# Kernel tuning notes

Hardware: AMD Instinct MI355X
Metric: run time of the kernel (lower is better)

Reference implementation:

```python
import jax, jax.numpy as jnp
import numpy as np

B, T, D = 2, 2048, 1024
H, DH = 16, 64
WINDOW = 256
SCALE = DH ** -0.5


def setup_inputs() -> dict:
    key = jax.random.key(0)
    ks = jax.random.split(key, 5)
    x = jax.random.normal(ks[0], (B, T, D), dtype=jnp.float32)
    # Linear params (y = x @ W + b form)
    w_qkv = jax.random.normal(ks[1], (D, 3 * D), dtype=jnp.float32) * (D ** -0.5)
    b_qkv = jnp.zeros((3 * D,), dtype=jnp.float32)
    w_out = jax.random.normal(ks[2], (D, D), dtype=jnp.float32) * (D ** -0.5)
    b_out = jnp.zeros((D,), dtype=jnp.float32)
    return {"x": x, "w_qkv": w_qkv, "b_qkv": b_qkv, "w_out": w_out, "b_out": b_out}


def reference(x, w_qkv, b_qkv, w_out, b_out):
    Bs, Ts, Ds = x.shape
    qkv = x @ w_qkv + b_qkv  # [B,T,3D]
    q, k, v = jnp.split(qkv, 3, axis=-1)
    # [B,H,T,dh]
    def heads(t):
        return t.reshape(Bs, Ts, H, DH).transpose(0, 2, 1, 3)
    q, k, v = heads(q), heads(k), heads(v)
    scores = jnp.einsum('bhqd,bhkd->bhqk', q, k) * SCALE
    i = jnp.arange(Ts)[:, None]
    j = jnp.arange(Ts)[None, :]
    # allowed: i - WINDOW <= j <= i  (causal + local window)
    allowed = (j <= i) & (j >= i - WINDOW)
    scores = jnp.where(allowed, scores, -jnp.inf)
    attn = jax.nn.softmax(scores, axis=-1)  # dropout is identity in eval
    out = jnp.einsum('bhqk,bhkd->bhqd', attn, v)
    out = out.transpose(0, 2, 1, 3).reshape(Bs, Ts, Ds)
    return out @ w_out + b_out
```

## Files before the change

### kernel.cpp

```cpp
#include <hip/hip_runtime.h>

#define BN 2
#define T_DIM 2048
#define D_DIM 1024
#define H_N 16
#define DH_N 64
#define WIN 256
#define NROWS (BN * T_DIM)
#define KDIM 1024

typedef __attribute__((ext_vector_type(8))) short bf16x8;
typedef __attribute__((ext_vector_type(4))) float f32x4;
typedef __attribute__((ext_vector_type(8))) unsigned short ushort8;
typedef __attribute__((ext_vector_type(4))) unsigned short u16x4;

static __device__ __forceinline__ unsigned short f2bf(float f) {
  unsigned int u = __float_as_uint(f);
  unsigned int r = (u + 0x7FFFu + ((u >> 16) & 1u)) >> 16;
  return (unsigned short)r;
}

static __device__ __forceinline__ void gl_lds16(const void* g, void* l) {
  __builtin_amdgcn_global_load_lds(
      (const __attribute__((address_space(1))) unsigned int*)g,
      (__attribute__((address_space(3))) unsigned int*)l, 16, 0, 0);
}

#define MFMA16(a, b, c) __builtin_amdgcn_mfma_f32_16x16x32_bf16(a, b, c, 0, 0, 0)

static __device__ __forceinline__ void transpose_tile(
    const float* __restrict__ src, unsigned short* __restrict__ dst, int R,
    int C, int bx, int by, float* tile ) {
  const int t = threadIdx.x;
  const int bc = bx * 64, br = by * 64;
#pragma unroll
  for (int i = 0; i < 16; ++i) {
    int idx = i * 256 + t;
    int r = idx >> 6, c = idx & 63;
    tile[r * 65 + c] = src[(size_t)(br + r) * C + bc + c];
  }
  __syncthreads();
#pragma unroll
  for (int i = 0; i < 16; ++i) {
    int idx = i * 256 + t;
    int r = idx >> 6, c = idx & 63;
    dst[(size_t)(bc + r) * R + br + c] = f2bf(tile[c * 65 + r]);
  }
}

__global__ __launch_bounds__(256) void convert_all(
    const float* __restrict__ x, const float* __restrict__ w_qkv,
    const float* __restrict__ w_out, unsigned short* __restrict__ xbf,
    unsigned short* __restrict__ wqkvt, unsigned short* __restrict__ woutt) {
  __shared__ float tile[64 * 65];
  const int id = blockIdx.x;
  if (id < 2048) {
    int i = (id * 256 + threadIdx.x) * 8;
    float4 a = *(const float4*)(x + i);
    float4 b = *(const float4*)(x + i + 4);
    ushort8 o;
    o[0] = f2bf(a.x); o[1] = f2bf(a.y); o[2] = f2bf(a.z); o[3] = f2bf(a.w);
    o[4] = f2bf(b.x); o[5] = f2bf(b.y); o[6] = f2bf(b.z); o[7] = f2bf(b.w);
    *(ushort8*)(xbf + i) = o;
  } else if (id < 2816) {
    int j = id - 2048;
    transpose_tile(w_qkv, wqkvt, D_DIM, 3 * D_DIM, j % 48, j / 48, tile);
  } else {
    int j = id - 2816;
    transpose_tile(w_out, woutt, D_DIM, D_DIM, j % 16, j / 16, tile);
  }
}

__global__ __launch_bounds__(512) void gemm_qkv_8p(
    const unsigned short* __restrict__ A, const unsigned short* __restrict__ Bt,
    const float* __restrict__ bias, unsigned short* __restrict__ qo,
    unsigned short* __restrict__ ko, unsigned short* __restrict__ vto) {
  __shared__ unsigned short As[2][256 * 64];
  __shared__ unsigned short Bs[2][192 * 64];

  const int tid = threadIdx.x;
  const int w = tid >> 6, l = tid & 63;
  const int wr = w >> 2, wc = w & 3;
  const int l15 = l & 15, kslc = l >> 4;

  const int id = blockIdx.x;
  const int wg = (id & 7) * 32 + (id >> 3);
  const int bx = wg & 15, by = wg >> 4;
  const int r0 = by * 256, c0 = bx * 192;

  const unsigned short* Ag = A + (size_t)r0 * KDIM;
  const unsigned short* Bg = Bt + (size_t)c0 * KDIM;

  f32x4 acc[8][3];
#pragma unroll
  for (int i = 0; i < 8; ++i)
#pragma unroll
    for (int j = 0; j < 3; ++j) acc[i][j] = (f32x4){0.f, 0.f, 0.f, 0.f};

  const int grow = tid >> 3;
  const int gcol = (tid & 7) ^ (grow & 7);

#define STAGE_A(T, BUF, CH)                                                    \
  gl_lds16(Ag + (size_t)((CH)*64 + grow) * KDIM + (T)*64 + gcol * 8,           \
           (char*)&As[BUF][0] + (CH)*8192 + w * 1024)
#define STAGE_B(T, BUF, CH)                                                    \
  gl_lds16(Bg + (size_t)((CH)*64 + grow) * KDIM + (T)*64 + gcol * 8,           \
           (char*)&Bs[BUF][0] + (CH)*8192 + w * 1024)

#define LDA(CB, mi, ks)                                                        \
  (*(const bf16x8*)((const char*)&As[CB][0] +                                  \
                    (wr * 128 + (mi)*16 + l15) * 128 +                         \
                    ((((ks)*4 + kslc) ^ (l15 & 7)) << 4)))
#define LDB(CB, ni, ks)                                                        \
  (*(const bf16x8*)((const char*)&Bs[CB][0] +                                  \
                    (wc * 48 + (ni)*16 + l15) * 128 +                          \
                    ((((ks)*4 + kslc) ^ (l15 & 7)) << 4)))

#define CLUSTER12(B_, A0, A1, A2, A3, B0, B1, B2)                              \
  do {                                                                         \
    __builtin_amdgcn_s_setprio(1);                                             \
    acc[B_ + 0][0] = MFMA16(A0, B0, acc[B_ + 0][0]);                           \
    acc[B_ + 0][1] = MFMA16(A0, B1, acc[B_ + 0][1]);                           \
    acc[B_ + 0][2] = MFMA16(A0, B2, acc[B_ + 0][2]);                           \
    acc[B_ + 1][0] = MFMA16(A1, B0, acc[B_ + 1][0]);                           \
    acc[B_ + 1][1] = MFMA16(A1, B1, acc[B_ + 1][1]);                           \
    acc[B_ + 1][2] = MFMA16(A1, B2, acc[B_ + 1][2]);                           \
    acc[B_ + 2][0] = MFMA16(A2, B0, acc[B_ + 2][0]);                           \
    acc[B_ + 2][1] = MFMA16(A2, B1, acc[B_ + 2][1]);                           \
    acc[B_ + 2][2] = MFMA16(A2, B2, acc[B_ + 2][2]);                           \
    acc[B_ + 3][0] = MFMA16(A3, B0, acc[B_ + 3][0]);                           \
    acc[B_ + 3][1] = MFMA16(A3, B1, acc[B_ + 3][1]);                           \
    acc[B_ + 3][2] = MFMA16(A3, B2, acc[B_ + 3][2]);                           \
    __builtin_amdgcn_s_setprio(0);                                             \
  } while (0)

  STAGE_A(0, 0, 0); STAGE_A(0, 0, 1); STAGE_A(0, 0, 2); STAGE_A(0, 0, 3);
  STAGE_B(0, 0, 0); STAGE_B(0, 0, 1); STAGE_B(0, 0, 2);

#pragma unroll 1
  for (int t = 0; t < 15; ++t) {
    const int cb = t & 1, nb = cb ^ 1;
    STAGE_A(t + 1, nb, 0); STAGE_A(t + 1, nb, 1);
    asm volatile("s_waitcnt vmcnt(2)" ::: "memory");
    __builtin_amdgcn_s_barrier();
    {
      bf16x8 a0 = LDA(cb, 0, 0), a1 = LDA(cb, 1, 0), a2 = LDA(cb, 2, 0),
             a3 = LDA(cb, 3, 0);
      bf16x8 b0 = LDB(cb, 0, 0), b1 = LDB(cb, 1, 0), b2 = LDB(cb, 2, 0);
      CLUSTER12(0, a0, a1, a2, a3, b0, b1, b2);
      __builtin_amdgcn_s_barrier();
      bf16x8 a4 = LDA(cb, 4, 0), a5 = LDA(cb, 5, 0), a6 = LDA(cb, 6, 0),
             a7 = LDA(cb, 7, 0);
      STAGE_A(t + 1, nb, 2); STAGE_A(t + 1, nb, 3);
      __builtin_amdgcn_s_barrier();
      CLUSTER12(4, a4, a5, a6, a7, b0, b1, b2);
      __builtin_amdgcn_s_barrier();
      bf16x8 c0_ = LDA(cb, 0, 1), c1_ = LDA(cb, 1, 1), c2_ = LDA(cb, 2, 1),
             c3_ = LDA(cb, 3, 1);
      bf16x8 d0 = LDB(cb, 0, 1), d1 = LDB(cb, 1, 1), d2 = LDB(cb, 2, 1);
      STAGE_B(t + 1, nb, 0); STAGE_B(t + 1, nb, 1);
      __builtin_amdgcn_s_barrier();
      CLUSTER12(0, c0_, c1_, c2_, c3_, d0, d1, d2);
      __builtin_amdgcn_s_barrier();
      bf16x8 c4 = LDA(cb, 4, 1), c5 = LDA(cb, 5, 1), c6 = LDA(cb, 6, 1),
             c7 = LDA(cb, 7, 1);
      STAGE_B(t + 1, nb, 2);
      __builtin_amdgcn_s_barrier();
      CLUSTER12(4, c4, c5, c6, c7, d0, d1, d2);
      __builtin_amdgcn_s_barrier();
    }
  }
  asm volatile("s_waitcnt vmcnt(0)" ::: "memory");
  __builtin_amdgcn_s_barrier();
  {
    bf16x8 a0 = LDA(1, 0, 0), a1 = LDA(1, 1, 0), a2 = LDA(1, 2, 0),
           a3 = LDA(1, 3, 0);
    bf16x8 b0 = LDB(1, 0, 0), b1 = LDB(1, 1, 0), b2 = LDB(1, 2, 0);
    CLUSTER12(0, a0, a1, a2, a3, b0, b1, b2);
    bf16x8 a4 = LDA(1, 4, 0), a5 = LDA(1, 5, 0), a6 = LDA(1, 6, 0),
           a7 = LDA(1, 7, 0);
    CLUSTER12(4, a4, a5, a6, a7, b0, b1, b2);
    bf16x8 c0_ = LDA(1, 0, 1), c1_ = LDA(1, 1, 1), c2_ = LDA(1, 2, 1),
           c3_ = LDA(1, 3, 1);
    bf16x8 d0 = LDB(1, 0, 1), d1 = LDB(1, 1, 1), d2 = LDB(1, 2, 1);
    CLUSTER12(0, c0_, c1_, c2_, c3_, d0, d1, d2);
    bf16x8 c4 = LDA(1, 4, 1), c5 = LDA(1, 5, 1), c6 = LDA(1, 6, 1),
           c7 = LDA(1, 7, 1);
    CLUSTER12(4, c4, c5, c6, c7, d0, d1, d2);
  }
#undef STAGE_A
#undef STAGE_B
#undef LDA
#undef LDB
#undef CLUSTER12

#pragma unroll
  for (int ni = 0; ni < 3; ++ni) {
    const int col0 = c0 + wc * 48 + ni * 16;
    const int which = col0 >> 10;
    const int h = (col0 >> 6) & 15;
    const int dh = (col0 & 63) + l15;
    const float bv = bias[col0 + l15];
#pragma unroll
    for (int mi = 0; mi < 8; ++mi) {
      int row = r0 + wr * 128 + mi * 16 + (l >> 4) * 4;
      int b_ = row >> 11, t0 = row & 2047;
      if (which == 2) {
        u16x4 pk;
#pragma unroll
        for (int j = 0; j < 4; ++j) pk[j] = f2bf(acc[mi][ni][j] + bv);
        *(u16x4*)(vto + ((size_t)(b_ * H_N + h) * DH_N + dh) * T_DIM + t0) = pk;
      } else {
        float mul = (which == 0) ? 0.125f : 1.0f;
        unsigned short* dst = (which == 0) ? qo : ko;
#pragma unroll
        for (int j = 0; j < 4; ++j)
          dst[((size_t)(b_ * H_N + h) * T_DIM + t0 + j) * DH_N + dh] =
              f2bf((acc[mi][ni][j] + bv) * mul);
      }
    }
  }
}

__global__ __launch_bounds__(256) void gemm_out_p4(
    const unsigned short* __restrict__ A, const unsigned short* __restrict__ Bt,
    const float* __restrict__ bias, float* __restrict__ fo) {
  __shared__ unsigned short As[4][4096];
  __shared__ unsigned short Bs[4][4096];

  const int tid = threadIdx.x;
  const int w = tid >> 6, l = tid & 63;
  const int wr = w >> 1, wc = w & 1;
  const int l15 = l & 15, kslc = l >> 4;

  const int id = blockIdx.x;
  const int wg = (id & 7) * 32 + (id >> 3);
  const int bx = wg & 7, by = wg >> 3;
  const int r0 = by * 128, c0 = bx * 128;

  const unsigned short* Ag = A + (size_t)r0 * KDIM;
  const unsigned short* Bg = Bt + (size_t)c0 * KDIM;

  f32x4 acc[4][4];
#pragma unroll
  for (int i = 0; i < 4; ++i)
#pragma unroll
    for (int j = 0; j < 4; ++j) acc[i][j] = (f32x4){0.f, 0.f, 0.f, 0.f};

  const int srow = l >> 2;
  const int srcslot = (l & 3) ^ ((l >> 3) & 3);

#define STAGE_O(T, BUF)                                                        \
  do {                                                                         \
    const size_t kk0 = (size_t)(T) * 32;                                       \
    gl_lds16(Ag + (size_t)(w * 16 + srow) * KDIM + kk0 + srcslot * 8,          \
             (char*)&As[BUF][0] + w * 1024);                                   \
    gl_lds16(Ag + (size_t)(64 + w * 16 + srow) * KDIM + kk0 + srcslot * 8,     \
             (char*)&As[BUF][0] + (4 + w) * 1024);                             \
    gl_lds16(Bg + (size_t)(w * 16 + srow) * KDIM + kk0 + srcslot * 8,          \
             (char*)&Bs[BUF][0] + w * 1024);                                   \
    gl_lds16(Bg + (size_t)(64 + w * 16 + srow) * KDIM + kk0 + srcslot * 8,     \
             (char*)&Bs[BUF][0] + (4 + w) * 1024);                             \
  } while (0)

#define OCOMPUTE(CB)                                                           \
  do {                                                                         \
    bf16x8 af[4], bfr[4];                                                      \
    _Pragma("unroll") for (int mi = 0; mi < 4; ++mi) {                         \
      int row = wr * 64 + mi * 16 + l15;                                       \
      af[mi] = *(const bf16x8*)((const char*)&As[CB][0] + row * 64 +           \
                                ((kslc ^ ((row >> 1) & 3)) << 4));             \
    }                                                                          \
    _Pragma("unroll") for (int ni = 0; ni < 4; ++ni) {                         \
      int row = wc * 64 + ni * 16 + l15;                                       \
      bfr[ni] = *(const bf16x8*)((const char*)&Bs[CB][0] + row * 64 +          \
                                 ((kslc ^ ((row >> 1) & 3)) << 4));            \
    }                                                                          \
    __builtin_amdgcn_s_setprio(1);                                             \
    _Pragma("unroll") for (int mi = 0; mi < 4; ++mi)                           \
        _Pragma("unroll") for (int ni = 0; ni < 4; ++ni) acc[mi][ni] =         \
            MFMA16(af[mi], bfr[ni], acc[mi][ni]);                              \
    __builtin_amdgcn_s_setprio(0);                                             \
  } while (0)

  STAGE_O(0, 0);
  STAGE_O(1, 1);

  for (int t = 0; t < 30; ++t) {
    STAGE_O(t + 2, (t + 2) & 3);
    asm volatile("s_waitcnt vmcnt(8)" ::: "memory");
    __builtin_amdgcn_s_barrier();
    OCOMPUTE(t & 3);
  }
  asm volatile("s_waitcnt vmcnt(4)" ::: "memory");
  __builtin_amdgcn_s_barrier();
  OCOMPUTE(2);
  asm volatile("s_waitcnt vmcnt(0)" ::: "memory");
  __builtin_amdgcn_s_barrier();
  OCOMPUTE(3);
#undef STAGE_O
#undef OCOMPUTE

#pragma unroll
  for (int mi = 0; mi < 4; ++mi) {
#pragma unroll
    for (int ni = 0; ni < 4; ++ni) {
      int row = r0 + wr * 64 + mi * 16 + (l >> 4) * 4;
      int col = c0 + wc * 64 + ni * 16 + l15;
      float bv = bias[col];
#pragma unroll
      for (int j = 0; j < 4; ++j)
        fo[(size_t)(row + j) * D_DIM + col] = acc[mi][ni][j] + bv;
    }
  }
}

__global__ __launch_bounds__(256) void attn_mono(
    const unsigned short* __restrict__ qbf,
    const unsigned short* __restrict__ kbf,
    const unsigned short* __restrict__ vtbf,
    unsigned short* __restrict__ ctx) {
  __shared__ unsigned short Ks[5 * 4096];
  __shared__ unsigned short Vs[5 * 4096];
  const int tid = threadIdx.x;
  const int w = tid >> 6, l = tid & 63;
  const int g = l >> 4, ln = l & 15;
  const int qt = blockIdx.x & 31;
  const int bh = blockIdx.x >> 5;
  const int q0 = qt * 64;
  const int q_abs = q0 + w * 16 + ln;

  const unsigned short* kp = kbf + (size_t)bh * T_DIM * DH_N;
  const unsigned short* vtp = vtbf + (size_t)bh * DH_N * T_DIM;

  bf16x8 qf0, qf1;
  {
    const unsigned short* qp = qbf + ((size_t)bh * T_DIM + q_abs) * DH_N;
    qf0 = *(const bf16x8*)(qp + g * 8);
    qf1 = *(const bf16x8*)(qp + 32 + g * 8);
  }

#define KAP(row) \
  (32 * (((row) >> 4) & 1) + 8 * (((row)&15) >> 2) + 4 * ((row) >> 5) + ((row)&3))

  const int kt_lo = (q0 >= WIN) ? (q0 - WIN) : 0;
  const int nt = ((q0 - kt_lo) >> 6) + 1;

  for (int i = 0; i < nt; ++i) {
    const int kt = kt_lo + i * 64;
#pragma unroll
    for (int i_ = 0; i_ < 2; ++i_) {
      int chunk = i_ * 256 + tid;
      int row = chunk >> 3, c16 = chunk & 7;
      int sc16 = c16 ^ (row & 7);
      int kap = KAP(row);
      gl_lds16(kp + (size_t)(kt + kap) * DH_N + sc16 * 8,
               (char*)Ks + i * 8192 + chunk * 16);
      gl_lds16(vtp + (size_t)row * T_DIM + kt + sc16 * 8,
               (char*)Vs + i * 8192 + chunk * 16);
    }
  }
  asm volatile("s_waitcnt vmcnt(0)" ::: "memory");
  __builtin_amdgcn_s_barrier();

  f32x4 acc_o[4];
#pragma unroll
  for (int nd = 0; nd < 4; ++nd) acc_o[nd] = (f32x4){0.f, 0.f, 0.f, 0.f};
  float m = -1e30f, lsum = 0.f;

  for (int i = 0; i < nt; ++i) {
    const int kt = kt_lo + i * 64;
    const char* Kb = (const char*)Ks + i * 8192;
    const char* Vb = (const char*)Vs + i * 8192;

    f32x4 sacc[4];
#pragma unroll
    for (int nk = 0; nk < 4; ++nk) sacc[nk] = (f32x4){0.f, 0.f, 0.f, 0.f};
#pragma unroll
    for (int ks = 0; ks < 2; ++ks) {
      bf16x8 qf = ks ? qf1 : qf0;
#pragma unroll
      for (int nk = 0; nk < 4; ++nk) {
        int rrow = nk * 16 + ln;
        int c16 = ks * 4 + g;
        bf16x8 kf =
            *(const bf16x8*)(Kb + rrow * 128 + ((c16 ^ (rrow & 7)) * 16));
        sacc[nk] = MFMA16(kf, qf, sacc[nk]);
      }
    }

    float p[4][4];
    float tm = -1e30f;
#pragma unroll
    for (int nk = 0; nk < 4; ++nk)
#pragma unroll
      for (int j = 0; j < 4; ++j) {
        int k_abs = kt + 32 * (nk & 1) + 8 * g + 4 * (nk >> 1) + j;
        float s = sacc[nk][j];
        bool ok = (k_abs <= q_abs) && (k_abs + WIN >= q_abs);
        s = ok ? s : -1e30f;
        p[nk][j] = s;
        tm = fmaxf(tm, s);
      }
    tm = fmaxf(tm, __shfl_xor(tm, 16, 64));
    tm = fmaxf(tm, __shfl_xor(tm, 32, 64));
    float mn = fmaxf(m, tm);
    float sc = __expf(m - mn);
    float ps = 0.f;
#pragma unroll
    for (int nk = 0; nk < 4; ++nk)
#pragma unroll
      for (int j = 0; j < 4; ++j) {
        p[nk][j] = __expf(p[nk][j] - mn);
        ps += p[nk][j];
      }
    ps += __shfl_xor(ps, 16, 64);
    ps += __shfl_xor(ps, 32, 64);
    lsum = lsum * sc + ps;
    m = mn;
#pragma unroll
    for (int nd = 0; nd < 4; ++nd) {
      acc_o[nd][0] *= sc; acc_o[nd][1] *= sc;
      acc_o[nd][2] *= sc; acc_o[nd][3] *= sc;
    }

    unsigned int pk[4][2];
#pragma unroll
    for (int nk = 0; nk < 4; ++nk) {
      pk[nk][0] = (unsigned)f2bf(p[nk][0]) | ((unsigned)f2bf(p[nk][1]) << 16);
      pk[nk][1] = (unsigned)f2bf(p[nk][2]) | ((unsigned)f2bf(p[nk][3]) << 16);
    }

#pragma unroll
    for (int ks = 0; ks < 2; ++ks) {
      union { unsigned int d[4]; bf16x8 v; } pf;
      pf.d[0] = pk[ks][0];     pf.d[1] = pk[ks][1];
      pf.d[2] = pk[2 + ks][0]; pf.d[3] = pk[2 + ks][1];
#pragma unroll
      for (int nd = 0; nd < 4; ++nd) {
        int drow = nd * 16 + ln;
        int c16 = ks * 4 + g;
        bf16x8 vf =
            *(const bf16x8*)(Vb + drow * 128 + ((c16 ^ (drow & 7)) * 16));
        acc_o[nd] = MFMA16(vf, pf.v, acc_o[nd]);
      }
    }
  }
#undef KAP

  float inv = 1.f / lsum;
  const int b_ = bh >> 4, h = bh & 15;
  unsigned short* op = ctx + ((size_t)b_ * T_DIM + q_abs) * D_DIM + h * DH_N;
#pragma unroll
  for (int nd = 0; nd < 4; ++nd) {
    u16x4 o;
#pragma unroll
    for (int j = 0; j < 4; ++j) o[j] = f2bf(acc_o[nd][j] * inv);
    *(u16x4*)(op + nd * 16 + g * 4) = o;
  }
}

extern "C" void kernel_launch(void* const* d_in, const int* in_sizes, int n_in,
                              void* d_out, int out_size, void* d_ws,
                              size_t ws_size, hipStream_t stream) {
  const float* x = (const float*)d_in[0];
  const float* w_qkv = (const float*)d_in[1];
  const float* b_qkv = (const float*)d_in[2];
  const float* w_out = (const float*)d_in[3];
  const float* b_out = (const float*)d_in[4];
  float* out = (float*)d_out;

  const size_t per = (size_t)BN * H_N * T_DIM * DH_N;
  unsigned short* qbf = (unsigned short*)d_ws;
  unsigned short* kbf = qbf + per;
  unsigned short* vtbf = kbf + per;
  unsigned short* xbf = vtbf + per;
  unsigned short* wqkvt = xbf + (size_t)NROWS * D_DIM;
  unsigned short* woutt = wqkvt + (size_t)3 * D_DIM * D_DIM;
  unsigned short* ctxbf = woutt + (size_t)D_DIM * D_DIM;

  convert_all<<<dim3(3072), dim3(256), 0, stream>>>(x, w_qkv, w_out, xbf,
                                                    wqkvt, woutt);

  gemm_qkv_8p<<<dim3(256), dim3(512), 0, stream>>>(xbf, wqkvt, b_qkv, qbf, kbf,
                                                   vtbf);

  attn_mono<<<dim3(BN * H_N * (T_DIM / 64)), dim3(256), 0, stream>>>(
      qbf, kbf, vtbf, ctxbf);

  gemm_out_p4<<<dim3(256), dim3(256), 0, stream>>>(ctxbf, woutt, b_out, out);
}
```

Measured before the change: 92.28 us.

## Load attention K/V fragments directly from global memory instead of LDS staging

The attention kernel no longer stages the whole K/V window into shared memory with a barrier. Each lane now reads its MFMA K and V^T fragments straight from global memory through precomputed per-lane base pointers. Block indices are also remapped so blocks with the same query tile but different heads run near each other, which should improve L2 locality. This frees LDS and removes the upfront load-and-wait, but every wave now issues its own global loads with no cross-wave reuse and no explicit prefetch, so it depends on cache hits.

Measured after the change: 109.4 us. 18.5% more time.

```diff
diff --git a/kernel.cpp b/kernel.cpp
--- a/kernel.cpp
+++ b/kernel.cpp
@@ -315,18 +315,19 @@
   }
 }
 
-__global__ __launch_bounds__(256) void attn_mono(
+__global__ __launch_bounds__(256) void attn_direct(
     const unsigned short* __restrict__ qbf,
     const unsigned short* __restrict__ kbf,
     const unsigned short* __restrict__ vtbf,
     unsigned short* __restrict__ ctx) {
-  __shared__ unsigned short Ks[5 * 4096];
-  __shared__ unsigned short Vs[5 * 4096];
   const int tid = threadIdx.x;
   const int w = tid >> 6, l = tid & 63;
   const int g = l >> 4, ln = l & 15;
-  const int qt = blockIdx.x & 31;
-  const int bh = blockIdx.x >> 5;
+
+  const int bid = blockIdx.x;
+  const int r_ = bid >> 3;
+  const int bh = (bid & 7) * 4 + (r_ & 3);
+  const int qt = r_ >> 2;
   const int q0 = qt * 64;
   const int q_abs = q0 + w * 16 + ln;
 
@@ -342,37 +343,25 @@
 
 #define KAP(row) \
   (32 * (((row) >> 4) & 1) + 8 * (((row)&15) >> 2) + 4 * ((row) >> 5) + ((row)&3))
-
-  const int kt_lo = (q0 >= WIN) ? (q0 - WIN) : 0;
-  const int nt = ((q0 - kt_lo) >> 6) + 1;
-
-  for (int i = 0; i < nt; ++i) {
-    const int kt = kt_lo + i * 64;
-#pragma unroll
-    for (int i_ = 0; i_ < 2; ++i_) {
-      int chunk = i_ * 256 + tid;
-      int row = chunk >> 3, c16 = chunk & 7;
-      int sc16 = c16 ^ (row & 7);
-      int kap = KAP(row);
-      gl_lds16(kp + (size_t)(kt + kap) * DH_N + sc16 * 8,
-               (char*)Ks + i * 8192 + chunk * 16);
-      gl_lds16(vtp + (size_t)row * T_DIM + kt + sc16 * 8,
-               (char*)Vs + i * 8192 + chunk * 16);
-    }
-  }
-  asm volatile("s_waitcnt vmcnt(0)" ::: "memory");
-  __builtin_amdgcn_s_barrier();
+  const unsigned short* kbase[4];
+#pragma unroll
+  for (int nk = 0; nk < 4; ++nk) {
+    int rrow = nk * 16 + ln;
+    kbase[nk] = kp + (size_t)KAP(rrow) * DH_N + g * 8;
+  }
+  const unsigned short* vbase[4];
+#pragma unroll
+  for (int nd = 0; nd < 4; ++nd)
+    vbase[nd] = vtp + (size_t)(nd * 16 + ln) * T_DIM + g * 8;
+#undef KAP
 
   f32x4 acc_o[4];
 #pragma unroll
   for (int nd = 0; nd < 4; ++nd) acc_o[nd] = (f32x4){0.f, 0.f, 0.f, 0.f};
   float m = -1e30f, lsum = 0.f;
 
-  for (int i = 0; i < nt; ++i) {
-    const int kt = kt_lo + i * 64;
-    const char* Kb = (const char*)Ks + i * 8192;
-    const char* Vb = (const char*)Vs + i * 8192;
-
+  const int kt_lo = (q0 >= WIN) ? (q0 - WIN) : 0;
+  for (int kt = kt_lo; kt <= q0; kt += 64) {
     f32x4 sacc[4];
 #pragma unroll
     for (int nk = 0; nk < 4; ++nk) sacc[nk] = (f32x4){0.f, 0.f, 0.f, 0.f};
@@ -381,10 +370,7 @@
       bf16x8 qf = ks ? qf1 : qf0;
 #pragma unroll
       for (int nk = 0; nk < 4; ++nk) {
-        int rrow = nk * 16 + ln;
-        int c16 = ks * 4 + g;
-        bf16x8 kf =
-            *(const bf16x8*)(Kb + rrow * 128 + ((c16 ^ (rrow & 7)) * 16));
+        bf16x8 kf = *(const bf16x8*)(kbase[nk] + (size_t)kt * DH_N + ks * 32);
         sacc[nk] = MFMA16(kf, qf, sacc[nk]);
       }
     }
@@ -438,15 +424,11 @@
       pf.d[2] = pk[2 + ks][0]; pf.d[3] = pk[2 + ks][1];
 #pragma unroll
       for (int nd = 0; nd < 4; ++nd) {
-        int drow = nd * 16 + ln;
-        int c16 = ks * 4 + g;
-        bf16x8 vf =
-            *(const bf16x8*)(Vb + drow * 128 + ((c16 ^ (drow & 7)) * 16));
+        bf16x8 vf = *(const bf16x8*)(vbase[nd] + kt + ks * 32);
         acc_o[nd] = MFMA16(vf, pf.v, acc_o[nd]);
       }
     }
   }
-#undef KAP
 
   float inv = 1.f / lsum;
   const int b_ = bh >> 4, h = bh & 15;
@@ -485,7 +467,7 @@
   gemm_qkv_8p<<<dim3(256), dim3(512), 0, stream>>>(xbf, wqkvt, b_qkv, qbf, kbf,
                                                    vtbf);
 
-  attn_mono<<<dim3(BN * H_N * (T_DIM / 64)), dim3(256), 0, stream>>>(
+  attn_direct<<<dim3(BN * H_N * (T_DIM / 64)), dim3(256), 0, stream>>>(
       qbf, kbf, vtbf, ctxbf);
 
   gemm_out_p4<<<dim3(256), dim3(256), 0, stream>>>(ctxbf, woutt, b_out, out);
```
